# Kernel optimization log

Hardware: AMD Instinct MI355X
Metric: run time of the kernel (lower is better)

The kernel has to match this reference:

```python
import jax, jax.numpy as jnp
import numpy as np

H = 70  # hidden size == input size


def _renorm_rows(w, max_norm=1.0, eps=1e-7):
    # emulate nn.Embedding(max_norm=1.0): clip row L2 norm to <= 1
    n = jnp.linalg.norm(w, axis=-1, keepdims=True)
    return jnp.where(n > max_norm, w * (max_norm / (n + eps)), w)


def _lstm(x, w_ih, w_hh, b_ih, b_hh):
    # x: (B, T, H). PyTorch gate order: i, f, g, o.
    B = x.shape[0]
    xg = jnp.einsum('bth,gh->btg', x, w_ih) + (b_ih + b_hh)  # (B, T, 4H)
    def step(carry, xt):
        h, c = carry
        gates = xt + h @ w_hh.T  # (B, 4H)
        i, f, g, o = jnp.split(gates, 4, axis=-1)
        i = jax.nn.sigmoid(i); f = jax.nn.sigmoid(f)
        g = jnp.tanh(g); o = jax.nn.sigmoid(o)
        c = f * c + i * g
        h = o * jnp.tanh(c)
        return (h, c), h
    h0 = jnp.zeros((B, H), x.dtype)
    (_, _), hs = jax.lax.scan(step, (h0, h0), jnp.swapaxes(xg, 0, 1))
    return jnp.swapaxes(hs, 0, 1)  # (B, T, H)


def setup_inputs() -> dict:
    key = jax.random.key(0)
    ks = jax.random.split(key, 12)
    B, S, C = 128, 512, 1104
    s = 0.1
    return {
        'x': jax.random.uniform(ks[0], (B, S, C), jnp.float32),
        'embed_w': jax.random.normal(ks[1], (C, H), jnp.float32),
        'w_ih': jax.random.normal(ks[2], (4 * H, H), jnp.float32) * s,
        'w_hh': jax.random.normal(ks[3], (4 * H, H), jnp.float32) * s,
        'b_ih': jax.random.normal(ks[4], (4 * H,), jnp.float32) * s,
        'b_hh': jax.random.normal(ks[5], (4 * H,), jnp.float32) * s,
        'attn_w1': jax.random.normal(ks[6], (64, H), jnp.float32) * s,
        'attn_b1': jax.random.normal(ks[7], (64,), jnp.float32) * s,
        'attn_w2': jax.random.normal(ks[8], (1, 64), jnp.float32) * s,
        'attn_b2': jax.random.normal(ks[9], (1,), jnp.float32) * s,
        'fc_w': jax.random.normal(ks[10], (3, H), jnp.float32) * s,
        'fc_b': jax.random.normal(ks[11], (3,), jnp.float32) * s,
    }


def reference(x, embed_w, w_ih, w_hh, b_ih, b_hh, attn_w1, attn_b1, attn_w2, attn_b2, fc_w, fc_b):
    w = _renorm_rows(embed_w)                      # (C, H)
    # fused form of (x[...,None] * weight).sum(dim=2): plain GEMM
    e = jnp.einsum('bsc,ch->bsh', x, w)            # (B, S, H)
    out = _lstm(e, w_ih, w_hh, b_ih, b_hh)         # (B, S, H)
    # self-attention pooling
    energy = jax.nn.relu(out @ attn_w1.T + attn_b1) @ attn_w2.T + attn_b2  # (B,S,1)
    weights = jax.nn.softmax(energy[..., 0], axis=1)                        # (B,S)
    pooled = jnp.einsum('bsh,bs->bh', out, weights)                         # (B,H)
    # dropout is identity at eval
    logits = pooled @ fc_w.T + fc_b
    return jax.nn.softmax(logits, axis=1)
```

## Files before the change

kernel.cpp:

```cpp
#include <hip/hip_runtime.h>
#include <math.h>

#define HDIM 70
#define HPAD 72
#define GATES 280
#define NG 288
#define TLEN 512
#define BATCH 128
#define CDIM 1104
#define KW 1152
#define ROWS 65536

#define OFF_WRN   0
#define OFF_BIAS  77312
#define OFF_WCT   77632
#define OFF_XG    243520
#define OFF_HOUT  9418560
#define OFF_EN    14137152

typedef short short8 __attribute__((ext_vector_type(8)));
typedef float f32x4 __attribute__((ext_vector_type(4)));

__device__ __forceinline__ unsigned short f2bf(float f) {
    unsigned int u = __float_as_uint(f);
    u = (u + 0x7fffu + ((u >> 16) & 1u)) >> 16;
    return (unsigned short)u;
}
__device__ __forceinline__ float bf2f(unsigned short s) {
    return __uint_as_float(((unsigned int)s) << 16);
}

__global__ __launch_bounds__(64) void k_renorm(const float* __restrict__ w,
                                               float* __restrict__ wrn) {
    const int row = blockIdx.x;
    const int lane = threadIdx.x;
    const float* wr = w + row * HDIM;
    float v0 = wr[lane];
    float v1 = (lane < 6) ? wr[64 + lane] : 0.0f;
    float ss = v0 * v0 + v1 * v1;
    #pragma unroll
    for (int off = 32; off > 0; off >>= 1) ss += __shfl_down(ss, off);
    float tot = __shfl(ss, 0);
    float n = sqrtf(tot);
    float scale = (n > 1.0f) ? 1.0f / (n + 1e-7f) : 1.0f;
    wrn[row * HDIM + lane] = v0 * scale;
    if (lane < 6) wrn[row * HDIM + 64 + lane] = v1 * scale;
}

__global__ __launch_bounds__(256) void k_prep(const float* __restrict__ wrn,
                                              const float* __restrict__ w_ih,
                                              const float* __restrict__ b_ih,
                                              const float* __restrict__ b_hh,
                                              unsigned short* __restrict__ wcT,
                                              float* __restrict__ bias) {
    const int n = blockIdx.x;
    const int tid = threadIdx.x;
    float wr[HDIM];
    if (n < GATES) {
        #pragma unroll
        for (int h = 0; h < HDIM; ++h) wr[h] = w_ih[n * HDIM + h];
        if (tid == 0) bias[n] = b_ih[n] + b_hh[n];
    } else {
        #pragma unroll
        for (int h = 0; h < HDIM; ++h) wr[h] = 0.0f;
    }
    for (int c = tid; c < KW; c += 256) {
        float a = 0.0f;
        if (n < GATES && c < CDIM) {
            const float* wc = wrn + c * HDIM;
            #pragma unroll
            for (int h = 0; h < HDIM; ++h) a += wr[h] * wc[h];
        }
        wcT[(size_t)n * KW + c] = f2bf(a);
    }
}

__global__ __launch_bounds__(256, 2) void k_xg_gemm(const float* __restrict__ x,
                                                    const unsigned short* __restrict__ wcT,
                                                    const float* __restrict__ bias,
                                                    unsigned short* __restrict__ xg) {
    __shared__ __align__(16) unsigned short A_lds[128 * 72];
    __shared__ __align__(16) unsigned short B_lds[NG * 72];
    const int tid = threadIdx.x;
    const int lane = tid & 63;
    const int w = tid >> 6;
    const int mh = (w >> 1) * 64;
    const int nh = (w & 1) * 144;
    const int l15 = lane & 15;
    const int q = lane >> 4;
    const size_t rbase = (size_t)blockIdx.x * 128;

    f32x4 acc[4][9];
    #pragma unroll
    for (int mt = 0; mt < 4; ++mt)
        #pragma unroll
        for (int nt = 0; nt < 9; ++nt) acc[mt][nt] = (f32x4){0.f, 0.f, 0.f, 0.f};

    const int r_st = tid >> 1;
    const int kh_st = (tid & 1) * 32;

    for (int kc = 0; kc < 18; ++kc) {
        const int k0 = kc * 64;
        {
            const float* xr = x + (rbase + r_st) * (size_t)CDIM + k0 + kh_st;
            unsigned short* dst = &A_lds[r_st * 72 + kh_st];
            #pragma unroll
            for (int qq = 0; qq < 8; ++qq) {
                const int kk = k0 + kh_st + qq * 4;
                float4 v = make_float4(0.f, 0.f, 0.f, 0.f);
                if (kk < CDIM) v = *(const float4*)(xr + qq * 4);
                unsigned int lo = (unsigned int)f2bf(v.x) | ((unsigned int)f2bf(v.y) << 16);
                unsigned int hi = (unsigned int)f2bf(v.z) | ((unsigned int)f2bf(v.w) << 16);
                uint2 pv; pv.x = lo; pv.y = hi;
                *(uint2*)&dst[qq * 4] = pv;
            }
        }
        {
            #pragma unroll
            for (int p = 0; p < 9; ++p) {
                const int cid = tid + p * 256;
                const int n = cid >> 3;
                const int ko = (cid & 7) * 8;
                uint4 v = *(const uint4*)(wcT + (size_t)n * KW + k0 + ko);
                *(uint4*)&B_lds[n * 72 + ko] = v;
            }
        }
        __syncthreads();
        #pragma unroll
        for (int ks = 0; ks < 2; ++ks) {
            short8 a[4];
            short8 bfr[9];
            #pragma unroll
            for (int mt = 0; mt < 4; ++mt)
                a[mt] = *(const short8*)&A_lds[(mh + mt * 16 + l15) * 72 + ks * 32 + q * 8];
            #pragma unroll
            for (int nt = 0; nt < 9; ++nt)
                bfr[nt] = *(const short8*)&B_lds[(nh + nt * 16 + l15) * 72 + ks * 32 + q * 8];
            #pragma unroll
            for (int mt = 0; mt < 4; ++mt)
                #pragma unroll
                for (int nt = 0; nt < 9; ++nt)
                    acc[mt][nt] = __builtin_amdgcn_mfma_f32_16x16x32_bf16(a[mt], bfr[nt], acc[mt][nt], 0, 0, 0);
        }
        __syncthreads();
    }
    #pragma unroll
    for (int nt = 0; nt < 9; ++nt) {
        const int n_g = nh + nt * 16 + l15;
        if (n_g >= GATES) continue;
        const float bv = bias[n_g];
        #pragma unroll
        for (int mt = 0; mt < 4; ++mt) {
            #pragma unroll
            for (int r = 0; r < 4; ++r) {
                const size_t row = rbase + mh + mt * 16 + q * 4 + r;
                xg[row * GATES + n_g] = f2bf(acc[mt][nt][r] + bv);
            }
        }
    }
}

__device__ __forceinline__ float sigmoid_fast(float v) {
    return 1.0f / (1.0f + __expf(-v));
}

#define DPPF(x, ctrl) __int_as_float(__builtin_amdgcn_mov_dpp(__float_as_int(x), (ctrl), 0xF, 0xF, true))

#define PF 8
__global__ __launch_bounds__(192) void k_lstm(const unsigned short* __restrict__ xg,
                                              const float* __restrict__ w_hh,
                                              float* __restrict__ hout) {
    __shared__ __align__(16) float h_lds[2][HPAD];
    const int tid = threadIdx.x;
    const int b = blockIdx.x;
    const int jl = tid >> 1;
    const int kh = tid & 1;
    const bool jv = (jl < HDIM);

    const float s0 = kh ? 2.0f : 1.0f;
    const float m0 = kh ? 2.0f : 1.0f;
    const float c0 = kh ? -1.0f : 0.0f;

    float wr0[36], wr1[36], wr2[36], wr3[36];
    #pragma unroll
    for (int kk = 0; kk < 36; ++kk) {
        const int k = kh * 36 + kk;
        const bool kv = jv && (k < HDIM);
        const size_t base = (size_t)jl * HDIM + k;
        wr0[kk] = kv ? w_hh[base] : 0.0f;
        wr1[kk] = kv ? w_hh[1 * HDIM * HDIM + base] : 0.0f;
        wr2[kk] = kv ? w_hh[2 * HDIM * HDIM + base] : 0.0f;
        wr3[kk] = kv ? w_hh[3 * HDIM * HDIM + base] : 0.0f;
    }
    if (tid < 2 * HPAD) ((float*)h_lds)[tid] = 0.0f;
    float c_reg = 0.0f;

    const int jc = jv ? jl : 0;
    const unsigned short* xpA = xg + (size_t)b * TLEN * GATES + kh * 140 + jc;
    const unsigned short* xpB = xpA + 70;
    float xbA[PF], xbB[PF];
    #pragma unroll
    for (int i = 0; i < PF; ++i) {
        xbA[i] = bf2f(xpA[i * GATES]);
        xbB[i] = bf2f(xpB[i * GATES]);
    }
    __syncthreads();

    #pragma unroll 8
    for (int t = 0; t < TLEN; ++t) {
        const int slot = t & (PF - 1);
        const int cu = t & 1;
        const float uA = xbA[slot];
        const float uB = xbB[slot];
        const int tp = (t + PF) & (TLEN - 1);
        xbA[slot] = bf2f(xpA[tp * GATES]);
        xbB[slot] = bf2f(xpB[tp * GATES]);

        const f32x4* hp4 = (const f32x4*)&h_lds[cu][kh * 36];
        float a0 = 0.f, a1 = 0.f, a2 = 0.f, a3 = 0.f;
        #pragma unroll
        for (int qi = 0; qi < 9; ++qi) {
            f32x4 hv = hp4[qi];
            #pragma unroll
            for (int e = 0; e < 4; ++e) {
                const float hvv = hv[e];
                const int kk = qi * 4 + e;
                a0 = fmaf(hvv, wr0[kk], a0);
                a1 = fmaf(hvv, wr1[kk], a1);
                a2 = fmaf(hvv, wr2[kk], a2);
                a3 = fmaf(hvv, wr3[kk], a3);
            }
        }
        a0 += DPPF(a0, 0xB1); a1 += DPPF(a1, 0xB1);
        a2 += DPPF(a2, 0xB1); a3 += DPPF(a3, 0xB1);

        const float t0 = (kh ? a2 : a0) + uA;
        const float t1 = (kh ? a3 : a1) + uB;
        const float act0 = fmaf(m0, sigmoid_fast(s0 * t0), c0);
        const float act1 = sigmoid_fast(t1);

        const float i_v = DPPF(act0, 0xA0);
        const float f_v = DPPF(act1, 0xA0);
        const float g_v = DPPF(act0, 0xF5);
        const float o_v = DPPF(act1, 0xF5);

        c_reg = fmaf(f_v, c_reg, i_v * g_v);
        const float hn = o_v * fmaf(2.0f, sigmoid_fast(2.0f * c_reg), -1.0f);
        if (kh == 0 && jv) {
            h_lds[cu ^ 1][jl] = hn;
            hout[((size_t)b * TLEN + t) * HPAD + jl] = hn;
        }
        asm volatile("s_waitcnt lgkmcnt(0)" ::: "memory");
        __builtin_amdgcn_s_barrier();
        __builtin_amdgcn_sched_barrier(0);
    }
}

__global__ __launch_bounds__(256) void k_energy(const float* __restrict__ hout,
                                                const float* __restrict__ w1,
                                                const float* __restrict__ b1,
                                                const float* __restrict__ w2,
                                                const float* __restrict__ b2,
                                                float* __restrict__ energy) {
    const int lane = threadIdx.x & 63;
    const int wid = blockIdx.x * 4 + (threadIdx.x >> 6);
    float w1r[HPAD];
    #pragma unroll
    for (int c = 0; c < HDIM; ++c) w1r[c] = w1[lane * HDIM + c];
    w1r[70] = w1r[71] = 0.0f;
    const float b1v = b1[lane];
    const float w2v = w2[lane];
    const float b2v = b2[0];
    for (int row = wid; row < ROWS; row += 4096) {
        const float4* rp = (const float4*)(hout + (size_t)row * HPAD);
        float a0 = 0.f, a1 = 0.f, a2 = 0.f, a3 = 0.f;
        #pragma unroll
        for (int jj = 0; jj < 18; ++jj) {
            float4 v = rp[jj];
            a0 += v.x * w1r[4 * jj];
            a1 += v.y * w1r[4 * jj + 1];
            a2 += v.z * w1r[4 * jj + 2];
            a3 += v.w * w1r[4 * jj + 3];
        }
        float hid = fmaxf((a0 + a1) + (a2 + a3) + b1v, 0.0f) * w2v;
        #pragma unroll
        for (int off = 32; off > 0; off >>= 1) hid += __shfl_down(hid, off);
        if (lane == 0) energy[row] = hid + b2v;
    }
}

__global__ __launch_bounds__(128) void k_pool(const float* __restrict__ hout,
                                              const float* __restrict__ energy,
                                              const float* __restrict__ fc_w,
                                              const float* __restrict__ fc_b,
                                              float* __restrict__ outp) {
    __shared__ float red[128];
    __shared__ float wexp[TLEN];
    __shared__ float pooledL[HDIM];
    const int tid = threadIdx.x;
    const int b = blockIdx.x;
    float v[4];
    #pragma unroll
    for (int k = 0; k < 4; ++k) v[k] = energy[b * TLEN + tid + 128 * k];
    float m = fmaxf(fmaxf(v[0], v[1]), fmaxf(v[2], v[3]));
    red[tid] = m; __syncthreads();
    for (int s = 64; s > 0; s >>= 1) {
        if (tid < s) red[tid] = fmaxf(red[tid], red[tid + s]);
        __syncthreads();
    }
    const float M = red[0]; __syncthreads();
    float s4 = 0.f;
    #pragma unroll
    for (int k = 0; k < 4; ++k) {
        float ex = __expf(v[k] - M);
        wexp[tid + 128 * k] = ex;
        s4 += ex;
    }
    red[tid] = s4; __syncthreads();
    for (int s = 64; s > 0; s >>= 1) {
        if (tid < s) red[tid] += red[tid + s];
        __syncthreads();
    }
    const float rinv = 1.0f / red[0];
    if (tid < HDIM) {
        float a0 = 0.f, a1 = 0.f, a2 = 0.f, a3 = 0.f;
        const float* hp = hout + (size_t)b * TLEN * HPAD + tid;
        for (int s = 0; s < TLEN; s += 4) {
            a0 += wexp[s]     * hp[(size_t)(s)     * HPAD];
            a1 += wexp[s + 1] * hp[(size_t)(s + 1) * HPAD];
            a2 += wexp[s + 2] * hp[(size_t)(s + 2) * HPAD];
            a3 += wexp[s + 3] * hp[(size_t)(s + 3) * HPAD];
        }
        pooledL[tid] = ((a0 + a1) + (a2 + a3)) * rinv;
    }
    __syncthreads();
    if (tid == 0) {
        float l[3];
        #pragma unroll
        for (int i = 0; i < 3; ++i) {
            float a = fc_b[i];
            for (int h = 0; h < HDIM; ++h) a += fc_w[i * HDIM + h] * pooledL[h];
            l[i] = a;
        }
        float m3 = fmaxf(l[0], fmaxf(l[1], l[2]));
        float e0 = __expf(l[0] - m3), e1 = __expf(l[1] - m3), e2 = __expf(l[2] - m3);
        float rs = 1.0f / (e0 + e1 + e2);
        outp[b * 3 + 0] = e0 * rs;
        outp[b * 3 + 1] = e1 * rs;
        outp[b * 3 + 2] = e2 * rs;
    }
}

extern "C" void kernel_launch(void* const* d_in, const int* in_sizes, int n_in,
                              void* d_out, int out_size, void* d_ws, size_t ws_size,
                              hipStream_t stream) {
    const float* x       = (const float*)d_in[0];
    const float* embed_w = (const float*)d_in[1];
    const float* w_ih    = (const float*)d_in[2];
    const float* w_hh    = (const float*)d_in[3];
    const float* b_ih    = (const float*)d_in[4];
    const float* b_hh    = (const float*)d_in[5];
    const float* aw1     = (const float*)d_in[6];
    const float* ab1     = (const float*)d_in[7];
    const float* aw2     = (const float*)d_in[8];
    const float* ab2     = (const float*)d_in[9];
    const float* fc_w    = (const float*)d_in[10];
    const float* fc_b    = (const float*)d_in[11];
    float* outp = (float*)d_out;
    float* ws = (float*)d_ws;

    float* wrn  = ws + OFF_WRN;
    float* bias = ws + OFF_BIAS;
    unsigned short* wcT = (unsigned short*)(ws + OFF_WCT);
    unsigned short* xgp = (unsigned short*)(ws + OFF_XG);
    float* ho = ws + OFF_HOUT;
    float* en = ws + OFF_EN;

    k_renorm<<<CDIM, 64, 0, stream>>>(embed_w, wrn);
    k_prep<<<NG, 256, 0, stream>>>(wrn, w_ih, b_ih, b_hh, wcT, bias);
    k_xg_gemm<<<512, 256, 0, stream>>>(x, wcT, bias, xgp);
    k_lstm<<<BATCH, 192, 0, stream>>>(xgp, w_hh, ho);
    k_energy<<<1024, 256, 0, stream>>>(ho, aw1, ab1, aw2, ab2, en);
    k_pool<<<BATCH, 128, 0, stream>>>(ho, en, fc_w, fc_b, outp);
}
```

Baseline: 824.3 us.

## Add producer wavefront streaming xg into LDS ring and writing hout

The LSTM recurrence kernel gains a fourth wavefront that prefetches upcoming timesteps' gate pre-activations from global memory into a 16-slot LDS ring buffer, two steps ahead. The same wavefront writes the previous step's hidden state from LDS to global. The compute wavefronts no longer issue per-step global loads or stores, which takes memory latency off the serial critical path. The cost is an extra wave per block that takes part in every per-step barrier, plus LDS ring traffic.

```diff
diff --git a/kernel.cpp b/kernel.cpp
--- a/kernel.cpp
+++ b/kernel.cpp
@@ -166,93 +166,117 @@
 
 #define DPPF(x, ctrl) __int_as_float(__builtin_amdgcn_mov_dpp(__float_as_int(x), (ctrl), 0xF, 0xF, true))
 
-#define PF 8
-__global__ __launch_bounds__(192) void k_lstm(const unsigned short* __restrict__ xg,
-                                              const float* __restrict__ w_hh,
-                                              float* __restrict__ hout) {
+#define RB 16
+__global__ __launch_bounds__(256, 1) void k_lstm(const unsigned short* __restrict__ xg,
+                                                 const float* __restrict__ w_hh,
+                                                 float* __restrict__ hout) {
     __shared__ __align__(16) float h_lds[2][HPAD];
+    __shared__ __align__(16) unsigned short ring[RB * GATES];
     const int tid = threadIdx.x;
     const int b = blockIdx.x;
+    const unsigned short* xgb = xg + (size_t)b * TLEN * GATES;
+
     const int jl = tid >> 1;
     const int kh = tid & 1;
     const bool jv = (jl < HDIM);
+    const int jc = jv ? jl : 0;
+    const int goff = kh * 140 + jc;
 
     const float s0 = kh ? 2.0f : 1.0f;
     const float m0 = kh ? 2.0f : 1.0f;
     const float c0 = kh ? -1.0f : 0.0f;
 
     float wr0[36], wr1[36], wr2[36], wr3[36];
-    #pragma unroll
-    for (int kk = 0; kk < 36; ++kk) {
-        const int k = kh * 36 + kk;
-        const bool kv = jv && (k < HDIM);
-        const size_t base = (size_t)jl * HDIM + k;
-        wr0[kk] = kv ? w_hh[base] : 0.0f;
-        wr1[kk] = kv ? w_hh[1 * HDIM * HDIM + base] : 0.0f;
-        wr2[kk] = kv ? w_hh[2 * HDIM * HDIM + base] : 0.0f;
-        wr3[kk] = kv ? w_hh[3 * HDIM * HDIM + base] : 0.0f;
-    }
-    if (tid < 2 * HPAD) ((float*)h_lds)[tid] = 0.0f;
+    uint4 r0, r1;
+    const int lane = tid - 192;
+
+    if (tid < 192) {
+        #pragma unroll
+        for (int kk = 0; kk < 36; ++kk) {
+            const int k = kh * 36 + kk;
+            const bool kv = jv && (k < HDIM);
+            const size_t base = (size_t)jl * HDIM + k;
+            wr0[kk] = kv ? w_hh[base] : 0.0f;
+            wr1[kk] = kv ? w_hh[1 * HDIM * HDIM + base] : 0.0f;
+            wr2[kk] = kv ? w_hh[2 * HDIM * HDIM + base] : 0.0f;
+            wr3[kk] = kv ? w_hh[3 * HDIM * HDIM + base] : 0.0f;
+        }
+        if (tid < 2 * HPAD) ((float*)h_lds)[tid] = 0.0f;
+    } else {
+        for (int c = lane; c < 490; c += 64) {
+            uint4 v = *(const uint4*)(xgb + c * 8);
+            *(uint4*)&ring[c * 8] = v;
+        }
+        if (lane < 35) {
+            r0 = *(const uint4*)(xgb + 14 * GATES + lane * 8);
+            r1 = *(const uint4*)(xgb + 15 * GATES + lane * 8);
+        }
+    }
     float c_reg = 0.0f;
-
-    const int jc = jv ? jl : 0;
-    const unsigned short* xpA = xg + (size_t)b * TLEN * GATES + kh * 140 + jc;
-    const unsigned short* xpB = xpA + 70;
-    float xbA[PF], xbB[PF];
-    #pragma unroll
-    for (int i = 0; i < PF; ++i) {
-        xbA[i] = bf2f(xpA[i * GATES]);
-        xbB[i] = bf2f(xpB[i * GATES]);
-    }
     __syncthreads();
 
     #pragma unroll 8
     for (int t = 0; t < TLEN; ++t) {
-        const int slot = t & (PF - 1);
-        const int cu = t & 1;
-        const float uA = xbA[slot];
-        const float uB = xbB[slot];
-        const int tp = (t + PF) & (TLEN - 1);
-        xbA[slot] = bf2f(xpA[tp * GATES]);
-        xbB[slot] = bf2f(xpB[tp * GATES]);
-
-        const f32x4* hp4 = (const f32x4*)&h_lds[cu][kh * 36];
-        float a0 = 0.f, a1 = 0.f, a2 = 0.f, a3 = 0.f;
-        #pragma unroll
-        for (int qi = 0; qi < 9; ++qi) {
-            f32x4 hv = hp4[qi];
-            #pragma unroll
-            for (int e = 0; e < 4; ++e) {
-                const float hvv = hv[e];
-                const int kk = qi * 4 + e;
-                a0 = fmaf(hvv, wr0[kk], a0);
-                a1 = fmaf(hvv, wr1[kk], a1);
-                a2 = fmaf(hvv, wr2[kk], a2);
-                a3 = fmaf(hvv, wr3[kk], a3);
-            }
-        }
-        a0 += DPPF(a0, 0xB1); a1 += DPPF(a1, 0xB1);
-        a2 += DPPF(a2, 0xB1); a3 += DPPF(a3, 0xB1);
-
-        const float t0 = (kh ? a2 : a0) + uA;
-        const float t1 = (kh ? a3 : a1) + uB;
-        const float act0 = fmaf(m0, sigmoid_fast(s0 * t0), c0);
-        const float act1 = sigmoid_fast(t1);
-
-        const float i_v = DPPF(act0, 0xA0);
-        const float f_v = DPPF(act1, 0xA0);
-        const float g_v = DPPF(act0, 0xF5);
-        const float o_v = DPPF(act1, 0xF5);
-
-        c_reg = fmaf(f_v, c_reg, i_v * g_v);
-        const float hn = o_v * fmaf(2.0f, sigmoid_fast(2.0f * c_reg), -1.0f);
-        if (kh == 0 && jv) {
-            h_lds[cu ^ 1][jl] = hn;
-            hout[((size_t)b * TLEN + t) * HPAD + jl] = hn;
+        if (tid < 192) {
+            const int slot = t & (RB - 1);
+            const float uA = bf2f(ring[slot * GATES + goff]);
+            const float uB = bf2f(ring[slot * GATES + goff + 70]);
+
+            const f32x4* hp4 = (const f32x4*)&h_lds[t & 1][kh * 36];
+            float a0 = 0.f, a1 = 0.f, a2 = 0.f, a3 = 0.f;
+            #pragma unroll
+            for (int qi = 0; qi < 9; ++qi) {
+                f32x4 hv = hp4[qi];
+                #pragma unroll
+                for (int e = 0; e < 4; ++e) {
+                    const float hvv = hv[e];
+                    const int kk = qi * 4 + e;
+                    a0 = fmaf(hvv, wr0[kk], a0);
+                    a1 = fmaf(hvv, wr1[kk], a1);
+                    a2 = fmaf(hvv, wr2[kk], a2);
+                    a3 = fmaf(hvv, wr3[kk], a3);
+                }
+            }
+            a0 += DPPF(a0, 0xB1); a1 += DPPF(a1, 0xB1);
+            a2 += DPPF(a2, 0xB1); a3 += DPPF(a3, 0xB1);
+
+            const float t0 = (kh ? a2 : a0) + uA;
+            const float t1 = (kh ? a3 : a1) + uB;
+            const float act0 = fmaf(m0, sigmoid_fast(s0 * t0), c0);
+            const float act1 = sigmoid_fast(t1);
+
+            const float i_v = DPPF(act0, 0xA0);
+            const float f_v = DPPF(act1, 0xA0);
+            const float g_v = DPPF(act0, 0xF5);
+            const float o_v = DPPF(act1, 0xF5);
+
+            c_reg = fmaf(f_v, c_reg, i_v * g_v);
+            const float hn = o_v * fmaf(2.0f, sigmoid_fast(2.0f * c_reg), -1.0f);
+            if (kh == 0 && jv) h_lds[(t + 1) & 1][jl] = hn;
+        } else {
+            if ((t & 1) == 0) {
+                if (lane < 35 && t + 14 < TLEN)
+                    *(uint4*)&ring[((t + 14) & (RB - 1)) * GATES + lane * 8] = r0;
+                if (lane < 35 && t + 16 < TLEN)
+                    r0 = *(const uint4*)(xgb + (size_t)(t + 16) * GATES + lane * 8);
+            } else {
+                if (lane < 35 && t + 14 < TLEN)
+                    *(uint4*)&ring[((t + 14) & (RB - 1)) * GATES + lane * 8] = r1;
+                if (lane < 35 && t + 16 < TLEN)
+                    r1 = *(const uint4*)(xgb + (size_t)(t + 16) * GATES + lane * 8);
+            }
+            if (lane < 35 && t >= 1) {
+                float2 hv = *(const float2*)&h_lds[t & 1][lane * 2];
+                *(float2*)&hout[((size_t)b * TLEN + (t - 1)) * HPAD + lane * 2] = hv;
+            }
         }
         asm volatile("s_waitcnt lgkmcnt(0)" ::: "memory");
         __builtin_amdgcn_s_barrier();
         __builtin_amdgcn_sched_barrier(0);
+    }
+    if (tid >= 192 && lane < 35) {
+        float2 hv = *(const float2*)&h_lds[0][lane * 2];
+        *(float2*)&hout[((size_t)b * TLEN + (TLEN - 1)) * HPAD + lane * 2] = hv;
     }
 }
 
@@ -379,7 +403,7 @@
     k_renorm<<<CDIM, 64, 0, stream>>>(embed_w, wrn);
     k_prep<<<NG, 256, 0, stream>>>(wrn, w_ih, b_ih, b_hh, wcT, bias);
     k_xg_gemm<<<512, 256, 0, stream>>>(x, wcT, bias, xgp);
-    k_lstm<<<BATCH, 192, 0, stream>>>(xgp, w_hh, ho);
+    k_lstm<<<BATCH, 256, 0, stream>>>(xgp, w_hh, ho);
     k_energy<<<1024, 256, 0, stream>>>(ho, aw1, ab1, aw2, ab2, en);
     k_pool<<<BATCH, 128, 0, stream>>>(ho, en, fc_w, fc_b, outp);
 }
```

After: 829.3 us. Within noise of the previous version (+0.6%).
